# Kernel tuning notes

Hardware: AMD Instinct MI355X
Metric: run time of the kernel (lower is better)

## Reference

```python
import jax, jax.numpy as jnp
import numpy as np
from functools import partial

C = 256
N_HEADS = 8
OFFSET_RANGE = 2.0


def _dwconv(x, w):
    # depthwise conv, SAME padding; w: (C,1,k,k)
    c = x.shape[1]
    return jax.lax.conv_general_dilated(
        x, w, window_strides=(1, 1), padding='SAME',
        feature_group_count=c, dimension_numbers=('NCHW', 'OIHW', 'NCHW'))


def _grid_sample_bilinear(x, gx, gy):
    # x: (B,C,H,W); gx,gy: (B,H,W) normalized in [-1,1]; align_corners=True
    B, Cc, H, W = x.shape
    ix = (gx + 1.0) * 0.5 * (W - 1)
    iy = (gy + 1.0) * 0.5 * (H - 1)
    x0f = jnp.floor(ix)
    y0f = jnp.floor(iy)
    fx = (ix - x0f)[:, None, :, :].reshape(B, 1, H * W)
    fy = (iy - y0f)[:, None, :, :].reshape(B, 1, H * W)
    x0 = jnp.clip(x0f.astype(jnp.int32), 0, W - 1)
    x1 = jnp.clip(x0 + 1, 0, W - 1)
    y0 = jnp.clip(y0f.astype(jnp.int32), 0, H - 1)
    y1 = jnp.clip(y0 + 1, 0, H - 1)
    xf = x.reshape(B, Cc, H * W)

    def gather(yi, xi):
        idx = (yi * W + xi).reshape(B, H * W)
        return jax.vmap(lambda f, i: f[:, i])(xf, idx)  # (B,C,N)

    v00 = gather(y0, x0)
    v01 = gather(y0, x1)
    v10 = gather(y1, x0)
    v11 = gather(y1, x1)
    out = (v00 * (1 - fx) * (1 - fy) + v01 * fx * (1 - fy)
           + v10 * (1 - fx) * fy + v11 * fx * fy)
    return out.reshape(B, Cc, H, W)


def setup_inputs() -> dict:
    key = jax.random.key(0)
    ks = jax.random.split(key, 11)
    B, H, W = 1, 64, 64
    s = 0.05
    return {
        'x': jax.random.normal(ks[0], (B, C, H, W), jnp.float32),
        'offset_weights': jnp.ones((3,), jnp.float32) + 0.1 * jax.random.normal(ks[1], (3,)),
        'w3': s * jax.random.normal(ks[2], (C, 1, 3, 3), jnp.float32),
        'w5': s * jax.random.normal(ks[3], (C, 1, 5, 5), jnp.float32),
        'w7': s * jax.random.normal(ks[4], (C, 1, 7, 7), jnp.float32),
        'w_offproj': s * jax.random.normal(ks[5], (2, C), jnp.float32),
        'wq': s * jax.random.normal(ks[6], (C, C), jnp.float32),
        'wk': s * jax.random.normal(ks[7], (C, C), jnp.float32),
        'wv': s * jax.random.normal(ks[8], (C, C), jnp.float32),
        'wo': s * jax.random.normal(ks[9], (C, C), jnp.float32),
        'beta': jnp.asarray(0.5, jnp.float32),
    }


def reference(x, offset_weights, w3, w5, w7, w_offproj, wq, wk, wv, wo, beta):
    B, Cc, H, W = x.shape
    head_dim = Cc // N_HEADS
    scale = head_dim ** -0.5
    N = H * W

    # multi-scale depthwise offset features
    off_feat = (_dwconv(x, w3) * offset_weights[0]
                + _dwconv(x, w5) * offset_weights[1]
                + _dwconv(x, w7) * offset_weights[2])
    offset = jnp.einsum('oc,bchw->bohw', w_offproj, jax.nn.relu(off_feat))  # (B,2,H,W) = (y,x)

    # reference points: ((i+0.5)/(size-1))*2 - 1
    ref_y = ((jnp.arange(H, dtype=jnp.float32) + 0.5) / (H - 1.0)) * 2.0 - 1.0
    ref_x = ((jnp.arange(W, dtype=jnp.float32) + 0.5) / (W - 1.0)) * 2.0 - 1.0
    gy = jnp.clip(ref_y[None, :, None] + jnp.tanh(offset[:, 0]) * OFFSET_RANGE, -1.0, 1.0)
    gx = jnp.clip(ref_x[None, None, :] + jnp.tanh(offset[:, 1]) * OFFSET_RANGE, -1.0, 1.0)
    x_sampled = _grid_sample_bilinear(x, gx, gy)

    # Manhattan decay bias
    yy = jnp.repeat(jnp.arange(H), W)
    xx = jnp.tile(jnp.arange(W), H)
    dist = (jnp.abs(yy[:, None] - yy[None, :]) + jnp.abs(xx[:, None] - xx[None, :])).astype(jnp.float32)
    decay = jnp.exp(-dist / (jnp.abs(beta) + 1e-6))  # (N,N)

    q = jnp.einsum('oc,bchw->bohw', wq, x).reshape(B, N_HEADS, head_dim, N)
    k = jnp.einsum('oc,bchw->bohw', wk, x_sampled).reshape(B, N_HEADS, head_dim, N)
    v = jnp.einsum('oc,bchw->bohw', wv, x_sampled).reshape(B, N_HEADS, head_dim, N)

    attn = jnp.einsum('bhdn,bhdm->bhnm', q, k) * scale + decay[None, None]
    attn = jax.nn.softmax(attn, axis=-1)
    out = jnp.einsum('bhnm,bhdm->bhdn', attn, v).reshape(B, Cc, H, W)
    return jnp.einsum('oc,bchw->bohw', wo, out)
```

## Files before the change

kernel.cpp:

```cpp
#include <hip/hip_runtime.h>
#include <hip/hip_bf16.h>


typedef __bf16 bf16x8 __attribute__((ext_vector_type(8)));
typedef float f32x4 __attribute__((ext_vector_type(4)));

__device__ __forceinline__ f32x4 mfma16(bf16x8 a, bf16x8 b, f32x4 c) {
    return __builtin_amdgcn_mfma_f32_16x16x32_bf16(a, b, c, 0, 0, 0);
}

__device__ __forceinline__ unsigned pack_bf16(float pa, float pb) {
    return __builtin_amdgcn_perm(__float_as_uint(pb), __float_as_uint(pa), 0x07060302u);
}

__global__ void transpose_kernel(const float* __restrict__ x,
                                 float* __restrict__ xTf,
                                 __hip_bfloat16* __restrict__ xTb) {
    __shared__ float tile[32][33];
    const int p0 = blockIdx.x * 32, c0 = blockIdx.y * 32;
    const int tx = threadIdx.x, ty = threadIdx.y;
#pragma unroll
    for (int i = 0; i < 4; ++i)
        tile[ty + i * 8][tx] = x[(size_t)(c0 + ty + i * 8) * 4096 + p0 + tx];
    __syncthreads();
#pragma unroll
    for (int i = 0; i < 4; ++i) {
        const float v = tile[tx][ty + i * 8];
        const size_t o = (size_t)(p0 + ty + i * 8) * 256 + c0 + tx;
        xTf[o] = v;
        xTb[o] = __float2bfloat16(v);
    }
}

__global__ void prep_kernel(const float* __restrict__ w3, const float* __restrict__ w5,
                            const float* __restrict__ w7, const float* __restrict__ ow,
                            const float* __restrict__ wq, const float* __restrict__ wk,
                            const float* __restrict__ wv, const float* __restrict__ wo,
                            float* __restrict__ wcomb, __hip_bfloat16* __restrict__ wb) {
    const int b = blockIdx.x;
    if (b < 49) {
        const int i = b, c = threadIdx.x;
        const int dy = i / 7, dx = i % 7;
        float val = ow[2] * w7[c * 49 + i];
        if (dy >= 1 && dy <= 5 && dx >= 1 && dx <= 5)
            val += ow[1] * w5[c * 25 + (dy - 1) * 5 + (dx - 1)];
        if (dy >= 2 && dy <= 4 && dx >= 2 && dx <= 4)
            val += ow[0] * w3[c * 9 + (dy - 2) * 3 + (dx - 2)];
        wcomb[i * 256 + c] = val;
    } else {
        const int idx = (b - 49) * 256 + threadIdx.x;
        const int m = idx >> 16;
        const float* src = (m == 0) ? wq : (m == 1) ? wk : (m == 2) ? wv : wo;
        const float sc = (m == 0) ? 0.25507535f : 1.0f;
        wb[idx] = __float2bfloat16(src[idx & 65535] * sc);
    }
}

__global__ __launch_bounds__(256) void sample_kernel(
    const float* __restrict__ xTf, const float* __restrict__ wcomb,
    const float* __restrict__ wop, __hip_bfloat16* __restrict__ xsT) {
    const int b = blockIdx.x;
    const int y = b >> 3;
    const int x0 = (b & 7) * 8;
    const int c = threadIdx.x;

    float wc[49];
#pragma unroll
    for (int i = 0; i < 49; ++i) wc[i] = wcomb[i * 256 + c];

    float acc[8];
#pragma unroll
    for (int px = 0; px < 8; ++px) acc[px] = 0.f;

#pragma unroll
    for (int dy = 0; dy < 7; ++dy) {
        const int yy = y + dy - 3;
        if (yy < 0 || yy > 63) continue;
        float v[14];
#pragma unroll
        for (int j = 0; j < 14; ++j) {
            const int xx = x0 - 3 + j;
            v[j] = (xx >= 0 && xx <= 63) ? xTf[(size_t)(yy * 64 + xx) * 256 + c] : 0.f;
        }
#pragma unroll
        for (int px = 0; px < 8; ++px)
#pragma unroll
            for (int dx = 0; dx < 7; ++dx)
                acc[px] = fmaf(v[px + dx], wc[dy * 7 + dx], acc[px]);
    }

    const float wy = wop[c], wx = wop[256 + c];
    float s[16];
#pragma unroll
    for (int px = 0; px < 8; ++px) {
        const float r = fmaxf(acc[px], 0.f);
        s[px] = wy * r;
        s[8 + px] = wx * r;
    }
#pragma unroll
    for (int off = 1; off < 64; off <<= 1)
#pragma unroll
        for (int i = 0; i < 16; ++i) s[i] += __shfl_xor(s[i], off, 64);

    __shared__ float red[4][16];
    const int lane = c & 63, wid = c >> 6;
    if (lane == 0)
#pragma unroll
        for (int i = 0; i < 16; ++i) red[wid][i] = s[i];
    __syncthreads();

#pragma unroll
    for (int px = 0; px < 8; ++px) {
        const float offy = red[0][px] + red[1][px] + red[2][px] + red[3][px];
        const float offx = red[0][8 + px] + red[1][8 + px] + red[2][8 + px] + red[3][8 + px];
        const int pxa = x0 + px;
        const float refy = ((y + 0.5f) / 63.0f) * 2.0f - 1.0f;
        const float refx = ((pxa + 0.5f) / 63.0f) * 2.0f - 1.0f;
        const float gy = fminf(fmaxf(refy + tanhf(offy) * 2.0f, -1.0f), 1.0f);
        const float gx = fminf(fmaxf(refx + tanhf(offx) * 2.0f, -1.0f), 1.0f);
        const float iy = (gy + 1.0f) * 31.5f;
        const float ix = (gx + 1.0f) * 31.5f;
        const float y0f = floorf(iy), x0f = floorf(ix);
        const float fy = iy - y0f, fx = ix - x0f;
        int yi0 = min(max((int)y0f, 0), 63), xi0 = min(max((int)x0f, 0), 63);
        int yi1 = min(yi0 + 1, 63), xi1 = min(xi0 + 1, 63);
        const float v00 = xTf[(size_t)(yi0 * 64 + xi0) * 256 + c];
        const float v01 = xTf[(size_t)(yi0 * 64 + xi1) * 256 + c];
        const float v10 = xTf[(size_t)(yi1 * 64 + xi0) * 256 + c];
        const float v11 = xTf[(size_t)(yi1 * 64 + xi1) * 256 + c];
        const float out = v00 * (1.f - fx) * (1.f - fy) + v01 * fx * (1.f - fy) +
                          v10 * (1.f - fx) * fy + v11 * fx * fy;
        xsT[(size_t)(y * 64 + pxa) * 256 + c] = __float2bfloat16(out);
    }
}

template <typename OutT>
__device__ __forceinline__ void gemm_body(const __hip_bfloat16* A, const __hip_bfloat16* B,
                                          OutT* out, int ldc, int m0, int n0) {
    const int w = threadIdx.x >> 6, lane = threadIdx.x & 63;
    const int g = lane >> 4, c = lane & 15;
    f32x4 acc[4];
#pragma unroll
    for (int nt = 0; nt < 4; ++nt) acc[nt] = (f32x4){0.f, 0.f, 0.f, 0.f};
    const __hip_bfloat16* Ar = A + (size_t)(m0 + w * 16 + c) * 256 + g * 8;
#pragma unroll
    for (int kc = 0; kc < 8; ++kc) {
        const bf16x8 a = *reinterpret_cast<const bf16x8*>(Ar + kc * 32);
#pragma unroll
        for (int nt = 0; nt < 4; ++nt) {
            const bf16x8 b = *reinterpret_cast<const bf16x8*>(
                B + (size_t)(n0 + nt * 16 + c) * 256 + kc * 32 + g * 8);
            acc[nt] = mfma16(a, b, acc[nt]);
        }
    }
#pragma unroll
    for (int nt = 0; nt < 4; ++nt)
#pragma unroll
        for (int r = 0; r < 4; ++r) {
            const size_t o = (size_t)(m0 + w * 16 + 4 * g + r) * ldc + n0 + nt * 16 + c;
            if constexpr (__is_same(OutT, float)) out[o] = acc[nt][r];
            else out[o] = __float2bfloat16(acc[nt][r]);
        }
}

__global__ __launch_bounds__(256) void gemm_qkv(const __hip_bfloat16* __restrict__ xq,
                                                const __hip_bfloat16* __restrict__ xs,
                                                const __hip_bfloat16* __restrict__ wb,
                                                __hip_bfloat16* __restrict__ q_t,
                                                __hip_bfloat16* __restrict__ k_t,
                                                __hip_bfloat16* __restrict__ vv) {
    const int z = blockIdx.z;
    if (z == 0)
        gemm_body<__hip_bfloat16>(xq, wb, q_t, 256, blockIdx.x * 64, blockIdx.y * 64);
    else if (z == 1)
        gemm_body<__hip_bfloat16>(xs, wb + 65536, k_t, 256, blockIdx.x * 64, blockIdx.y * 64);
    else
        gemm_body<__hip_bfloat16>(wb + 2 * 65536, xs, vv, 4096, blockIdx.y * 64,
                                  blockIdx.x * 64);
}

template <typename OutT>
__global__ __launch_bounds__(256) void gemm_abt(const __hip_bfloat16* __restrict__ A,
                                                const __hip_bfloat16* __restrict__ B,
                                                OutT* __restrict__ out, int ldc) {
    gemm_body<OutT>(A, B, out, ldc, blockIdx.x * 64, blockIdx.y * 64);
}

__global__ __launch_bounds__(256, 2) void attn_kernel(
    const __hip_bfloat16* __restrict__ q_t,
    const __hip_bfloat16* __restrict__ k_t,
    const __hip_bfloat16* __restrict__ vv,
    const float* __restrict__ beta_p,
    __hip_bfloat16* __restrict__ att)
{
    __shared__ __align__(16) char smem[34816];
    const int h = blockIdx.y;
    const int nb = blockIdx.x;
    const int n0 = nb * 64;
    const int tid = threadIdx.x;
    const int w = tid >> 6, lane = tid & 63, g = lane >> 4, c = lane & 15;

    const float bta = fabsf(beta_p[0]) + 1e-6f;
    const float L2E = 1.4426950408889634f;
    const float c2 = L2E / bta;

    float d64d[7][4];
#pragma unroll
    for (int dlt = 0; dlt < 7; ++dlt)
#pragma unroll
        for (int r = 0; r < 4; ++r) {
            const int dd = 16 * (dlt - 3) + c - 4 * g - r;
            d64d[dlt][r] = L2E * exp2f(-c2 * fabsf((float)dd));
        }

    bf16x8 aq[4];
#pragma unroll
    for (int nt = 0; nt < 4; ++nt)
        aq[nt] = *reinterpret_cast<const bf16x8*>(
            q_t + (size_t)(n0 + nt * 16 + c) * 256 + h * 32 + g * 8);

    f32x4 o_acc[4][2];
    float l_part[4] = {0.f, 0.f, 0.f, 0.f};
#pragma unroll
    for (int nt = 0; nt < 4; ++nt) {
        o_acc[nt][0] = (f32x4){0.f, 0.f, 0.f, 0.f};
        o_acc[nt][1] = (f32x4){0.f, 0.f, 0.f, 0.f};
    }

    uint2* pl = (uint2*)smem + w * 1024;
    const int wbi = g * 16 + c;
    const int rb = (g >> 1) * 64 + (g & 1) * 32 + c;
    const f32x4 zf = (f32x4){0.f, 0.f, 0.f, 0.f};

    auto loadK = [&](int it, bf16x8* bk) {
        const size_t m0 = (size_t)(it * 4 + w) * 64;
#pragma unroll
        for (int mt = 0; mt < 4; ++mt)
            bk[mt] = *reinterpret_cast<const bf16x8*>(
                k_t + (m0 + mt * 16 + c) * 256 + h * 32 + g * 8);
    };
    auto loadV = [&](int it, bf16x8 (*bv)[2]) {
        const size_t m0 = (size_t)(it * 4 + w) * 64;
#pragma unroll
        for (int dt = 0; dt < 2; ++dt)
#pragma unroll
            for (int mc = 0; mc < 2; ++mc)
                bv[dt][mc] = *reinterpret_cast<const bf16x8*>(
                    vv + (size_t)(h * 32 + dt * 16 + c) * 4096 + m0 + mc * 32 + g * 8);
    };
    auto body = [&](int it, bf16x8* bk, bf16x8 (*bv)[2]) {
        const int ym = it * 4 + w;
        const float a2 = exp2f(-c2 * fabsf((float)(nb - ym)));
#pragma unroll
        for (int nt = 0; nt < 4; ++nt) {
            f32x4 s[4];
#pragma unroll
            for (int mt = 0; mt < 4; ++mt) s[mt] = mfma16(bk[mt], aq[nt], zf);
#pragma unroll
            for (int mt = 0; mt < 4; ++mt) {
                float p[4];
#pragma unroll
                for (int r = 0; r < 4; ++r)
                    p[r] = exp2f(fmaf(a2, d64d[nt - mt + 3][r], s[mt][r]));
                l_part[nt] += (p[0] + p[1]) + (p[2] + p[3]);
                pl[wbi + (nt * 4 + mt) * 64] = uint2{pack_bf16(p[0], p[1]),
                                                     pack_bf16(p[2], p[3])};
            }
        }
#pragma unroll
        for (int nt = 0; nt < 4; ++nt)
#pragma unroll
            for (int mc = 0; mc < 2; ++mc) {
                const int idx = rb + (nt * 4 + 2 * mc) * 64;
                union { uint2 u[2]; bf16x8 v; } t;
                t.u[0] = pl[idx];
                t.u[1] = pl[idx + 16];
                o_acc[nt][0] = mfma16(t.v, bv[0][mc], o_acc[nt][0]);
                o_acc[nt][1] = mfma16(t.v, bv[1][mc], o_acc[nt][1]);
            }
    };

    bf16x8 bkA[4], bkB[4], bvA[2][2], bvB[2][2];
    loadK(0, bkA);
    loadV(0, bvA);
#pragma unroll 1
    for (int it2 = 0; it2 < 8; ++it2) {
        loadK(2 * it2 + 1, bkB);
        loadV(2 * it2 + 1, bvB);
        body(2 * it2, bkA, bvA);
        if (it2 < 7) {
            loadK(2 * it2 + 2, bkA);
            loadV(2 * it2 + 2, bvA);
        }
        body(2 * it2 + 1, bkB, bvB);
    }

#pragma unroll
    for (int nt = 0; nt < 4; ++nt) {
        float v = l_part[nt];
        v += __shfl_xor(v, 16);
        v += __shfl_xor(v, 32);
        l_part[nt] = v;
    }

    __syncthreads();
    float* ob = (float*)smem;
    float* lred = (float*)(smem + 33792);
#pragma unroll
    for (int nt = 0; nt < 4; ++nt) {
        if (g == 0) lred[w * 64 + nt * 16 + c] = l_part[nt];
#pragma unroll
        for (int r = 0; r < 4; ++r) {
            const int row = 16 * nt + 4 * g + r;
            ob[w * 2112 + row * 33 + c] = o_acc[nt][0][r];
            ob[w * 2112 + row * 33 + 16 + c] = o_acc[nt][1][r];
        }
    }
    __syncthreads();

#pragma unroll
    for (int k = 0; k < 8; ++k) {
        const int flat = k * 256 + tid;
        const int row = flat >> 5, d = flat & 31;
        const float O = ob[row * 33 + d] + ob[2112 + row * 33 + d] +
                        ob[4224 + row * 33 + d] + ob[6336 + row * 33 + d];
        const float L = lred[row] + lred[64 + row] + lred[128 + row] + lred[192 + row];
        att[(size_t)(n0 + row) * 256 + h * 32 + d] = __float2bfloat16(O / L);
    }
}

extern "C" void kernel_launch(void* const* d_in, const int* in_sizes, int n_in,
                              void* d_out, int out_size, void* d_ws, size_t ws_size,
                              hipStream_t stream) {
    (void)in_sizes; (void)n_in; (void)out_size; (void)ws_size;
    const float* x    = (const float*)d_in[0];
    const float* ow   = (const float*)d_in[1];
    const float* w3   = (const float*)d_in[2];
    const float* w5   = (const float*)d_in[3];
    const float* w7   = (const float*)d_in[4];
    const float* wop  = (const float*)d_in[5];
    const float* wq   = (const float*)d_in[6];
    const float* wk   = (const float*)d_in[7];
    const float* wv   = (const float*)d_in[8];
    const float* wo   = (const float*)d_in[9];
    const float* beta = (const float*)d_in[10];

    char* ws = (char*)d_ws;
    const size_t MB = 1 << 20;
    float*          xTf = (float*)(ws);
    __hip_bfloat16* xTb = (__hip_bfloat16*)(ws + 4 * MB);
    __hip_bfloat16* xsT = (__hip_bfloat16*)(ws + 6 * MB);
    __hip_bfloat16* q_t = (__hip_bfloat16*)(ws + 8 * MB);
    __hip_bfloat16* k_t = (__hip_bfloat16*)(ws + 10 * MB);
    __hip_bfloat16* vv  = (__hip_bfloat16*)(ws + 12 * MB);
    __hip_bfloat16* att = (__hip_bfloat16*)(ws + 14 * MB);
    __hip_bfloat16* wb  = (__hip_bfloat16*)(ws + 16 * MB);
    float* wcomb        = (float*)(ws + 16 * MB + 512 * 1024);
    __hip_bfloat16* wob = wb + 3 * 65536;

    transpose_kernel<<<dim3(128, 8), dim3(32, 8), 0, stream>>>(x, xTf, xTb);
    prep_kernel<<<1073, 256, 0, stream>>>(w3, w5, w7, ow, wq, wk, wv, wo, wcomb, wb);
    sample_kernel<<<512, 256, 0, stream>>>(xTf, wcomb, wop, xsT);
    gemm_qkv<<<dim3(64, 4, 3), 256, 0, stream>>>(xTb, xsT, wb, q_t, k_t, vv);
    attn_kernel<<<dim3(64, 8), 256, 0, stream>>>(q_t, k_t, vv, beta, att);
    gemm_abt<float><<<dim3(4, 64), 256, 0, stream>>>(wob, att, (float*)d_out, 4096);
}
```

Baseline: 163.7 us.

## Merge transpose and prep kernels, compute softmax row sums via MFMA, use fast exp/tanh

Folds the transpose and weight-prep kernels into one launch, which removes a kernel launch. In attention, the softmax denominator is now accumulated with an extra MFMA against a ones vector instead of scalar adds plus cross-lane shuffles, and the reduction buffer padding changes from 33 to 36 floats. exp2f and tanhf are replaced with hardware exp2/rcp intrinsics. The trade-offs are one more MFMA per P·V step, slightly larger shared memory, and a normalizer summed from bf16-rounded probabilities, with a small loss of accuracy.

```diff
diff --git a/kernel.cpp b/kernel.cpp
--- a/kernel.cpp
+++ b/kernel.cpp
@@ -13,33 +13,36 @@
     return __builtin_amdgcn_perm(__float_as_uint(pb), __float_as_uint(pa), 0x07060302u);
 }
 
-__global__ void transpose_kernel(const float* __restrict__ x,
-                                 float* __restrict__ xTf,
-                                 __hip_bfloat16* __restrict__ xTb) {
+__device__ __forceinline__ float fast_tanh(float x) {
+    const float t = __builtin_amdgcn_exp2f(x * 2.8853900817779268f);
+    return (t - 1.0f) * __builtin_amdgcn_rcpf(t + 1.0f);
+}
+
+__global__ void prep_transpose_kernel(const float* __restrict__ x, float* __restrict__ xTf,
+                                      __hip_bfloat16* __restrict__ xTb,
+                                      const float* __restrict__ w3, const float* __restrict__ w5,
+                                      const float* __restrict__ w7, const float* __restrict__ ow,
+                                      const float* __restrict__ wq, const float* __restrict__ wk,
+                                      const float* __restrict__ wv, const float* __restrict__ wo,
+                                      float* __restrict__ wcomb, __hip_bfloat16* __restrict__ wb) {
     __shared__ float tile[32][33];
-    const int p0 = blockIdx.x * 32, c0 = blockIdx.y * 32;
-    const int tx = threadIdx.x, ty = threadIdx.y;
-#pragma unroll
-    for (int i = 0; i < 4; ++i)
-        tile[ty + i * 8][tx] = x[(size_t)(c0 + ty + i * 8) * 4096 + p0 + tx];
-    __syncthreads();
-#pragma unroll
-    for (int i = 0; i < 4; ++i) {
-        const float v = tile[tx][ty + i * 8];
-        const size_t o = (size_t)(p0 + ty + i * 8) * 256 + c0 + tx;
-        xTf[o] = v;
-        xTb[o] = __float2bfloat16(v);
-    }
-}
-
-__global__ void prep_kernel(const float* __restrict__ w3, const float* __restrict__ w5,
-                            const float* __restrict__ w7, const float* __restrict__ ow,
-                            const float* __restrict__ wq, const float* __restrict__ wk,
-                            const float* __restrict__ wv, const float* __restrict__ wo,
-                            float* __restrict__ wcomb, __hip_bfloat16* __restrict__ wb) {
     const int b = blockIdx.x;
-    if (b < 49) {
-        const int i = b, c = threadIdx.x;
+    if (b < 1024) {
+        const int p0 = (b >> 3) * 32, c0 = (b & 7) * 32;
+        const int tx = threadIdx.x & 31, ty = threadIdx.x >> 5;
+#pragma unroll
+        for (int i = 0; i < 4; ++i)
+            tile[ty + i * 8][tx] = x[(size_t)(c0 + ty + i * 8) * 4096 + p0 + tx];
+        __syncthreads();
+#pragma unroll
+        for (int i = 0; i < 4; ++i) {
+            const float v = tile[tx][ty + i * 8];
+            const size_t o = (size_t)(p0 + ty + i * 8) * 256 + c0 + tx;
+            xTf[o] = v;
+            xTb[o] = __float2bfloat16(v);
+        }
+    } else if (b < 1073) {
+        const int i = b - 1024, c = threadIdx.x;
         const int dy = i / 7, dx = i % 7;
         float val = ow[2] * w7[c * 49 + i];
         if (dy >= 1 && dy <= 5 && dx >= 1 && dx <= 5)
@@ -48,7 +51,7 @@
             val += ow[0] * w3[c * 9 + (dy - 2) * 3 + (dx - 2)];
         wcomb[i * 256 + c] = val;
     } else {
-        const int idx = (b - 49) * 256 + threadIdx.x;
+        const int idx = (b - 1073) * 256 + threadIdx.x;
         const int m = idx >> 16;
         const float* src = (m == 0) ? wq : (m == 1) ? wk : (m == 2) ? wv : wo;
         const float sc = (m == 0) ? 0.25507535f : 1.0f;
@@ -116,8 +119,8 @@
         const int pxa = x0 + px;
         const float refy = ((y + 0.5f) / 63.0f) * 2.0f - 1.0f;
         const float refx = ((pxa + 0.5f) / 63.0f) * 2.0f - 1.0f;
-        const float gy = fminf(fmaxf(refy + tanhf(offy) * 2.0f, -1.0f), 1.0f);
-        const float gx = fminf(fmaxf(refx + tanhf(offx) * 2.0f, -1.0f), 1.0f);
+        const float gy = fminf(fmaxf(refy + fast_tanh(offy) * 2.0f, -1.0f), 1.0f);
+        const float gx = fminf(fmaxf(refx + fast_tanh(offx) * 2.0f, -1.0f), 1.0f);
         const float iy = (gy + 1.0f) * 31.5f;
         const float ix = (gx + 1.0f) * 31.5f;
         const float y0f = floorf(iy), x0f = floorf(ix);
@@ -193,7 +196,7 @@
     const float* __restrict__ beta_p,
     __hip_bfloat16* __restrict__ att)
 {
-    __shared__ __align__(16) char smem[34816];
+    __shared__ __align__(16) char smem[37888];
     const int h = blockIdx.y;
     const int nb = blockIdx.x;
     const int n0 = nb * 64;
@@ -210,7 +213,7 @@
 #pragma unroll
         for (int r = 0; r < 4; ++r) {
             const int dd = 16 * (dlt - 3) + c - 4 * g - r;
-            d64d[dlt][r] = L2E * exp2f(-c2 * fabsf((float)dd));
+            d64d[dlt][r] = L2E * __builtin_amdgcn_exp2f(-c2 * fabsf((float)dd));
         }
 
     bf16x8 aq[4];
@@ -219,12 +222,16 @@
         aq[nt] = *reinterpret_cast<const bf16x8*>(
             q_t + (size_t)(n0 + nt * 16 + c) * 256 + h * 32 + g * 8);
 
-    f32x4 o_acc[4][2];
-    float l_part[4] = {0.f, 0.f, 0.f, 0.f};
+    bf16x8 ones;
+#pragma unroll
+    for (int j = 0; j < 8; ++j) ones[j] = (__bf16)1.0f;
+
+    f32x4 o_acc[4][2], l_acc[4];
 #pragma unroll
     for (int nt = 0; nt < 4; ++nt) {
         o_acc[nt][0] = (f32x4){0.f, 0.f, 0.f, 0.f};
         o_acc[nt][1] = (f32x4){0.f, 0.f, 0.f, 0.f};
+        l_acc[nt] = (f32x4){0.f, 0.f, 0.f, 0.f};
     }
 
     uint2* pl = (uint2*)smem + w * 1024;
@@ -250,7 +257,7 @@
     };
     auto body = [&](int it, bf16x8* bk, bf16x8 (*bv)[2]) {
         const int ym = it * 4 + w;
-        const float a2 = exp2f(-c2 * fabsf((float)(nb - ym)));
+        const float a2 = __builtin_amdgcn_exp2f(-c2 * fabsf((float)(nb - ym)));
 #pragma unroll
         for (int nt = 0; nt < 4; ++nt) {
             f32x4 s[4];
@@ -261,8 +268,7 @@
                 float p[4];
 #pragma unroll
                 for (int r = 0; r < 4; ++r)
-                    p[r] = exp2f(fmaf(a2, d64d[nt - mt + 3][r], s[mt][r]));
-                l_part[nt] += (p[0] + p[1]) + (p[2] + p[3]);
+                    p[r] = __builtin_amdgcn_exp2f(fmaf(a2, d64d[nt - mt + 3][r], s[mt][r]));
                 pl[wbi + (nt * 4 + mt) * 64] = uint2{pack_bf16(p[0], p[1]),
                                                      pack_bf16(p[2], p[3])};
             }
@@ -277,6 +283,7 @@
                 t.u[1] = pl[idx + 16];
                 o_acc[nt][0] = mfma16(t.v, bv[0][mc], o_acc[nt][0]);
                 o_acc[nt][1] = mfma16(t.v, bv[1][mc], o_acc[nt][1]);
+                l_acc[nt] = mfma16(t.v, ones, l_acc[nt]);
             }
     };
 
@@ -295,35 +302,26 @@
         body(2 * it2 + 1, bkB, bvB);
     }
 
-#pragma unroll
-    for (int nt = 0; nt < 4; ++nt) {
-        float v = l_part[nt];
-        v += __shfl_xor(v, 16);
-        v += __shfl_xor(v, 32);
-        l_part[nt] = v;
-    }
-
     __syncthreads();
     float* ob = (float*)smem;
-    float* lred = (float*)(smem + 33792);
-#pragma unroll
-    for (int nt = 0; nt < 4; ++nt) {
-        if (g == 0) lred[w * 64 + nt * 16 + c] = l_part[nt];
+    float* lred = (float*)(smem + 36864);
+#pragma unroll
+    for (int nt = 0; nt < 4; ++nt)
 #pragma unroll
         for (int r = 0; r < 4; ++r) {
             const int row = 16 * nt + 4 * g + r;
-            ob[w * 2112 + row * 33 + c] = o_acc[nt][0][r];
-            ob[w * 2112 + row * 33 + 16 + c] = o_acc[nt][1][r];
-        }
-    }
+            if (c == 0) lred[w * 64 + row] = l_acc[nt][r];
+            ob[w * 2304 + row * 36 + c] = o_acc[nt][0][r];
+            ob[w * 2304 + row * 36 + 16 + c] = o_acc[nt][1][r];
+        }
     __syncthreads();
 
 #pragma unroll
     for (int k = 0; k < 8; ++k) {
         const int flat = k * 256 + tid;
         const int row = flat >> 5, d = flat & 31;
-        const float O = ob[row * 33 + d] + ob[2112 + row * 33 + d] +
-                        ob[4224 + row * 33 + d] + ob[6336 + row * 33 + d];
+        const float O = ob[row * 36 + d] + ob[2304 + row * 36 + d] +
+                        ob[4608 + row * 36 + d] + ob[6912 + row * 36 + d];
         const float L = lred[row] + lred[64 + row] + lred[128 + row] + lred[192 + row];
         att[(size_t)(n0 + row) * 256 + h * 32 + d] = __float2bfloat16(O / L);
     }
@@ -358,8 +356,8 @@
     float* wcomb        = (float*)(ws + 16 * MB + 512 * 1024);
     __hip_bfloat16* wob = wb + 3 * 65536;
 
-    transpose_kernel<<<dim3(128, 8), dim3(32, 8), 0, stream>>>(x, xTf, xTb);
-    prep_kernel<<<1073, 256, 0, stream>>>(w3, w5, w7, ow, wq, wk, wv, wo, wcomb, wb);
+    prep_transpose_kernel<<<2097, 256, 0, stream>>>(x, xTf, xTb, w3, w5, w7, ow,
+                                                    wq, wk, wv, wo, wcomb, wb);
     sample_kernel<<<512, 256, 0, stream>>>(xTf, wcomb, wop, xsT);
     gemm_qkv<<<dim3(64, 4, 3), 256, 0, stream>>>(xTb, xsT, wb, q_t, k_t, vv);
     attn_kernel<<<dim3(64, 8), 256, 0, stream>>>(q_t, k_t, vv, beta, att);
```

Result: faster. 147.5 us (-9.9%).
